# Performance work log

Measured on AMD Instinct MI355X. Metric: run time of the kernel, lower is better.

Reference implementation:

```python
import jax, jax.numpy as jnp
import numpy as np

B, S, H, D = 2, 2048, 16, 64
DM = H * D  # d_model = 1024


def setup_inputs() -> dict:
    key = jax.random.key(0)
    ks = jax.random.split(key, 12)
    scale = 1.0 / np.sqrt(DM)
    inp = {
        "queries": jax.random.normal(ks[0], (B, S, DM), jnp.float32),
        "keys": jax.random.normal(ks[1], (B, S, DM), jnp.float32),
        "values": jax.random.normal(ks[2], (B, S, DM), jnp.float32),
        # binary (0/1) causal mask, broadcast to (B, H, S, S) as the torch API expects
        "mask": jnp.broadcast_to(jnp.tril(jnp.ones((S, S), jnp.float32)), (B, H, S, S)),
        "wq": jax.random.normal(ks[3], (DM, DM), jnp.float32) * scale,
        "bq": jax.random.normal(ks[4], (DM,), jnp.float32) * scale,
        "wk": jax.random.normal(ks[5], (DM, DM), jnp.float32) * scale,
        "bk": jax.random.normal(ks[6], (DM,), jnp.float32) * scale,
        "wv": jax.random.normal(ks[7], (DM, DM), jnp.float32) * scale,
        "bv": jax.random.normal(ks[8], (DM,), jnp.float32) * scale,
        "wy": jax.random.normal(ks[9], (DM, DM), jnp.float32) * scale,
        "by": jax.random.normal(ks[10], (DM,), jnp.float32) * scale,
    }
    return inp


def _split_heads(x):
    # (B, S, H*D) -> (B, H, S, D)
    b, s, _ = x.shape
    return x.reshape(b, s, H, D).transpose(0, 2, 1, 3)


def reference(queries, keys, values, mask, wq, bq, wk, bk, wv, bv, wy, by):
    # torch nn.Linear: y = x @ W^T + b
    q = _split_heads(queries @ wq.T + bq)  # (B, H, S, D)
    k = _split_heads(keys @ wk.T + bk)
    v = _split_heads(values @ wv.T + bv)

    s = jnp.einsum("bhqd,bhkd->bhqk", q, k) / jnp.sqrt(jnp.float32(D))
    # custom additive-multiplicative mask: s*mask - 1e4*(1-mask)
    s = s * mask - 1e4 * (1.0 - mask)
    w = jax.nn.softmax(s, axis=-1)
    av = jnp.einsum("bhqk,bhkd->bhqd", w, v)  # (B, H, S, D)
    y = av.transpose(0, 2, 1, 3).reshape(queries.shape[0], queries.shape[1], DM)
    return y @ wy.T + by
```

## Files before the change

kernel.cpp:

```cpp
#include <hip/hip_runtime.h>
#include <math.h>

#define BB 2
#define SS 2048
#define HH 16
#define DD 64
#define DMODEL 1024
#define MROWS (BB * SS)

typedef __attribute__((ext_vector_type(8))) short bf16x8;
typedef __attribute__((ext_vector_type(4))) float f32x4;

__device__ __forceinline__ f32x4 mfma16(bf16x8 a, bf16x8 b, f32x4 c) {
    return __builtin_amdgcn_mfma_f32_16x16x32_bf16(a, b, c, 0, 0, 0);
}

__device__ __forceinline__ unsigned short bf16_1(float x) {
    unsigned u = __builtin_bit_cast(unsigned, x);
    u += 0x7fffu + ((u >> 16) & 1u);
    return (unsigned short)(u >> 16);
}
__device__ __forceinline__ unsigned pack_bf16(float a, float b) {
    unsigned ua = __builtin_bit_cast(unsigned, a);
    unsigned ub = __builtin_bit_cast(unsigned, b);
    ua += 0x7fffu + ((ua >> 16) & 1u);
    ub += 0x7fffu + ((ub >> 16) & 1u);
    return (ua >> 16) | (ub & 0xffff0000u);
}

__global__ __launch_bounds__(256) void cvt_bf16(const float* __restrict__ q,
                                                const float* __restrict__ k,
                                                const float* __restrict__ v,
                                                const float* __restrict__ wq,
                                                const float* __restrict__ wk,
                                                const float* __restrict__ wv,
                                                const float* __restrict__ wy,
                                                unsigned short* __restrict__ dst)
{
    const size_t idx = ((size_t)blockIdx.x * 256 + threadIdx.x) * 8;
    const int mc = (int)(idx >> 20);
    const float* src; size_t off;
    if      (mc < 4)   { src = q;  off = idx; }
    else if (mc < 8)   { src = k;  off = idx - ((size_t)4  << 20); }
    else if (mc < 12)  { src = v;  off = idx - ((size_t)8  << 20); }
    else if (mc == 12) { src = wq; off = idx - ((size_t)12 << 20); }
    else if (mc == 13) { src = wk; off = idx - ((size_t)13 << 20); }
    else if (mc == 14) { src = wv; off = idx - ((size_t)14 << 20); }
    else               { src = wy; off = idx - ((size_t)15 << 20); }
    float4 a = *(const float4*)(src + off);
    float4 b = *(const float4*)(src + off + 4);
    uint4 o;
    o.x = pack_bf16(a.x, a.y); o.y = pack_bf16(a.z, a.w);
    o.z = pack_bf16(b.x, b.y); o.w = pack_bf16(b.z, b.w);
    *(uint4*)(dst + idx) = o;
}

template<int TM>
__device__ __forceinline__ void gemm_body(const unsigned short* __restrict__ A,
                                          const unsigned short* __restrict__ W,
                                          const float* __restrict__ bias,
                                          void* __restrict__ out,
                                          int a_mode, int out_mode)
{
    constexpr int NT  = (TM == 128) ? 4 : 2;
    constexpr int ACH = TM * 8;
    __shared__ int4 lds4[ACH + 1024];
    const int tid = threadIdx.x;
    const int w = tid >> 6, lane = tid & 63;
    const int L = lane & 15, Q = lane >> 4;
    const int m0 = blockIdx.x * TM;
    const int n0 = blockIdx.y * 128;
    const int wm = (TM == 128) ? (w & 1) * 64 : 0;
    const int wn = (TM == 128) ? (w >> 1) * 64 : w * 32;

    f32x4 acc[4][NT] = {};

    for (int c = 0; c < 16; ++c) {
        __syncthreads();
        #pragma unroll
        for (int i = 0; i < TM / 32; ++i) {
            int cid = tid + 256 * i;
            int row = cid >> 3, ch = cid & 7;
            int m = m0 + row;
            size_t gaddr;
            if (a_mode == 0) gaddr = (size_t)m * DMODEL + (size_t)c * 64 + ch * 8;
            else {
                int b = m >> 11, s = m & 2047;
                gaddr = (((size_t)b * HH + c) * SS + s) * DD + ch * 8;
            }
            lds4[row * 8 + (ch ^ (row & 7))] = *(const int4*)(A + gaddr);
        }
        #pragma unroll
        for (int i = 0; i < 4; ++i) {
            int cid = tid + 256 * i;
            int row = cid >> 3, ch = cid & 7;
            lds4[ACH + row * 8 + (ch ^ (row & 7))] =
                *(const int4*)(W + (size_t)(n0 + row) * DMODEL + (size_t)c * 64 + ch * 8);
        }
        __syncthreads();
        #pragma unroll
        for (int kf = 0; kf < 2; ++kf) {
            bf16x8 af[4], bfr[NT];
            #pragma unroll
            for (int mt = 0; mt < 4; ++mt) {
                int row = wm + 16 * mt + L;
                af[mt] = __builtin_bit_cast(bf16x8, lds4[row * 8 + ((Q + 4 * kf) ^ (row & 7))]);
            }
            #pragma unroll
            for (int nt = 0; nt < NT; ++nt) {
                int row = wn + 16 * nt + L;
                bfr[nt] = __builtin_bit_cast(bf16x8, lds4[ACH + row * 8 + ((Q + 4 * kf) ^ (row & 7))]);
            }
            #pragma unroll
            for (int mt = 0; mt < 4; ++mt)
                #pragma unroll
                for (int nt = 0; nt < NT; ++nt)
                    acc[mt][nt] = mfma16(af[mt], bfr[nt], acc[mt][nt]);
        }
    }

    #pragma unroll
    for (int mt = 0; mt < 4; ++mt)
        #pragma unroll
        for (int nt = 0; nt < NT; ++nt) {
            const int mbase = m0 + wm + 16 * mt + 4 * Q;
            const int n = n0 + wn + 16 * nt + L;
            float v0 = acc[mt][nt][0] + bias[n];
            float v1 = acc[mt][nt][1] + bias[n];
            float v2 = acc[mt][nt][2] + bias[n];
            float v3 = acc[mt][nt][3] + bias[n];
            if (out_mode == 1) {
                float* o = (float*)out + (size_t)mbase * DMODEL + n;
                o[0] = v0; o[DMODEL] = v1; o[2 * DMODEL] = v2; o[3 * DMODEL] = v3;
            } else if (out_mode == 0) {
                int b = mbase >> 11, s = mbase & 2047, h = n >> 6, d = n & 63;
                unsigned short* o = (unsigned short*)out + (((size_t)b * HH + h) * SS + s) * DD + d;
                o[0] = bf16_1(v0); o[DD] = bf16_1(v1); o[2 * DD] = bf16_1(v2); o[3 * DD] = bf16_1(v3);
            } else {
                int b = mbase >> 11, s = mbase & 2047, h = n >> 6, d = n & 63;
                uint2 p; p.x = pack_bf16(v0, v1); p.y = pack_bf16(v2, v3);
                *(uint2*)((unsigned short*)out + (((size_t)b * HH + h) * DD + d) * SS + s) = p;
            }
        }
}

__global__ __launch_bounds__(256) void qkv_gemm(const unsigned short* __restrict__ qcv,
                                                const unsigned short* __restrict__ kcv,
                                                const unsigned short* __restrict__ vcv,
                                                const unsigned short* __restrict__ wqb,
                                                const unsigned short* __restrict__ wkb,
                                                const unsigned short* __restrict__ wvb,
                                                const float* __restrict__ bq,
                                                const float* __restrict__ bk,
                                                const float* __restrict__ bv,
                                                unsigned short* __restrict__ qh,
                                                unsigned short* __restrict__ kh,
                                                unsigned short* __restrict__ vtb)
{
    const int z = blockIdx.z;
    const unsigned short* A = (z == 0) ? qcv : (z == 1) ? kcv : vcv;
    const unsigned short* W = (z == 0) ? wqb : (z == 1) ? wkb : wvb;
    const float* bias       = (z == 0) ? bq  : (z == 1) ? bk  : bv;
    unsigned short* out     = (z == 0) ? qh  : (z == 1) ? kh  : vtb;
    gemm_body<128>(A, W, bias, out, 0, (z == 2) ? 2 : 0);
}

__global__ __launch_bounds__(256) void out_gemm(const unsigned short* __restrict__ avb,
                                                const unsigned short* __restrict__ wyb,
                                                const float* __restrict__ by,
                                                float* __restrict__ out)
{
    gemm_body<64>(avb, wyb, by, out, 1, 1);
}

__global__ __launch_bounds__(256) void attn_mfma(const unsigned short* __restrict__ qb,
                                                 const unsigned short* __restrict__ kb,
                                                 const unsigned short* __restrict__ vt,
                                                 unsigned short* __restrict__ av)
{
    __shared__ int4 lds4[1536];
    const int tid  = threadIdx.x;
    const int w    = tid >> 6;
    const int lane = tid & 63;
    const int L = lane & 15, Q = lane >> 4;
    const int h = blockIdx.y, b = blockIdx.z;
    const size_t base = ((size_t)b * HH + h) * SS * DD;
    const float SC = 0.125f * 1.4426950408889634f;

    const int srcA = L + 32 * (Q & 1);
    const int srcB = srcA + 16;
    const bool hisel = (Q & 2) != 0;

    for (int pass = 0; pass < 2; ++pass) {
        const int qt  = pass ? (31 - (int)blockIdx.x) : (int)blockIdx.x;
        const int q0  = qt * 64;
        const int q0w = q0 + 16 * w;

        __syncthreads();
        #pragma unroll
        for (int i = 0; i < 2; ++i) {
            int cid = tid + 256 * i;
            int row = cid >> 3, ch = cid & 7;
            lds4[row * 8 + (ch ^ (row & 7))] =
                *(const int4*)(qb + base + (size_t)(q0 + row) * DD + ch * 8);
        }
        __syncthreads();

        bf16x8 qf[2];
        #pragma unroll
        for (int kf = 0; kf < 2; ++kf) {
            int row = 16 * w + L;
            qf[kf] = __builtin_bit_cast(bf16x8, lds4[row * 8 + ((Q + 4 * kf) ^ (row & 7))]);
        }

        float m2 = -1e30f, l2 = 0.f;
        f32x4 acc[4] = {};

        const int nkt = qt + 1;
        for (int kt = 0; kt < nkt; ++kt) {
            const int k0 = kt * 64;
            __syncthreads();
            #pragma unroll
            for (int i = 0; i < 2; ++i) {
                int cid = tid + 256 * i;
                int row = cid >> 3, ch = cid & 7;
                lds4[512 + row * 8 + (ch ^ (row & 7))] =
                    *(const int4*)(kb + base + (size_t)(k0 + row) * DD + ch * 8);
            }
            #pragma unroll
            for (int i = 0; i < 2; ++i) {
                int cid = tid + 256 * i;
                int row = cid >> 3, ch = cid & 7;
                lds4[1024 + row * 8 + (ch ^ (row & 7))] =
                    *(const int4*)(vt + base + (size_t)row * SS + k0 + ch * 8);
            }
            __syncthreads();

            f32x4 st[4] = {};
            #pragma unroll
            for (int kf = 0; kf < 2; ++kf) {
                bf16x8 kfr[4];
                #pragma unroll
                for (int rt = 0; rt < 4; ++rt) {
                    int row = 16 * rt + L;
                    kfr[rt] = __builtin_bit_cast(bf16x8, lds4[512 + row * 8 + ((Q + 4 * kf) ^ (row & 7))]);
                }
                #pragma unroll
                for (int rt = 0; rt < 4; ++rt)
                    st[rt] = mfma16(kfr[rt], qf[kf], st[rt]);
            }

            const bool need_mask = (k0 + 63 > q0w);
            const int qg = q0w + L;
            float mx = -1e30f;
            #pragma unroll
            for (int rt = 0; rt < 4; ++rt)
                #pragma unroll
                for (int r = 0; r < 4; ++r) {
                    float s = st[rt][r] * SC;
                    if (need_mask) {
                        int kg = k0 + 16 * rt + 4 * Q + r;
                        s = (kg > qg) ? -2e30f : s;
                    }
                    st[rt][r] = s;
                    mx = fmaxf(mx, s);
                }
            mx = fmaxf(mx, __shfl_xor(mx, 16, 64));
            mx = fmaxf(mx, __shfl_xor(mx, 32, 64));
            const float mn = fmaxf(m2, mx);
            const float alpha = exp2f(m2 - mn);
            m2 = mn;
            float ls = 0.f;
            unsigned pd[4][2];
            #pragma unroll
            for (int rt = 0; rt < 4; ++rt) {
                float p0 = exp2f(st[rt][0] - mn), p1 = exp2f(st[rt][1] - mn);
                float p2 = exp2f(st[rt][2] - mn), p3 = exp2f(st[rt][3] - mn);
                ls += (p0 + p1) + (p2 + p3);
                pd[rt][0] = pack_bf16(p0, p1);
                pd[rt][1] = pack_bf16(p2, p3);
            }
            ls += __shfl_xor(ls, 16, 64);
            ls += __shfl_xor(ls, 32, 64);
            l2 = l2 * alpha + ls;
            #pragma unroll
            for (int rt = 0; rt < 4; ++rt) acc[rt] *= alpha;

            #pragma unroll
            for (int kf = 0; kf < 2; ++kf) {
                bf16x8 vf[4];
                #pragma unroll
                for (int rt = 0; rt < 4; ++rt) {
                    int row = 16 * rt + L;
                    vf[rt] = __builtin_bit_cast(bf16x8, lds4[1024 + row * 8 + ((Q + 4 * kf) ^ (row & 7))]);
                }
                unsigned lo0 = pd[2 * kf + 0][0], lo1 = pd[2 * kf + 0][1];
                unsigned hi0 = pd[2 * kf + 1][0], hi1 = pd[2 * kf + 1][1];
                unsigned xa_lo0 = (unsigned)__shfl((int)lo0, srcA, 64);
                unsigned xa_lo1 = (unsigned)__shfl((int)lo1, srcA, 64);
                unsigned xb_lo0 = (unsigned)__shfl((int)lo0, srcB, 64);
                unsigned xb_lo1 = (unsigned)__shfl((int)lo1, srcB, 64);
                unsigned xa_hi0 = (unsigned)__shfl((int)hi0, srcA, 64);
                unsigned xa_hi1 = (unsigned)__shfl((int)hi1, srcA, 64);
                unsigned xb_hi0 = (unsigned)__shfl((int)hi0, srcB, 64);
                unsigned xb_hi1 = (unsigned)__shfl((int)hi1, srcB, 64);
                uint4 bw;
                bw.x = hisel ? xa_hi0 : xa_lo0;
                bw.y = hisel ? xa_hi1 : xa_lo1;
                bw.z = hisel ? xb_hi0 : xb_lo0;
                bw.w = hisel ? xb_hi1 : xb_lo1;
                bf16x8 pf = __builtin_bit_cast(bf16x8, bw);
                #pragma unroll
                for (int rt = 0; rt < 4; ++rt)
                    acc[rt] = mfma16(vf[rt], pf, acc[rt]);
            }
        }

        __syncthreads();
        {
            int4* ep4 = lds4 + w * 256;
            const float inv = 1.0f / l2;
            #pragma unroll
            for (int rt = 0; rt < 4; ++rt) {
                f32x4 ov = acc[rt] * inv;
                ep4[L * 16 + ((4 * rt + Q) ^ (L & 15))] = __builtin_bit_cast(int4, ov);
            }
        }
        __syncthreads();
        {
            uint2* epu = (uint2*)(lds4 + w * 256);
            #pragma unroll
            for (int i = 0; i < 8; ++i) {
                int pid = lane + 64 * i;
                int rr  = pid >> 5;
                int c   = pid & 31;
                uint2 f2 = epu[(rr * 16 + ((c >> 1) ^ (rr & 15))) * 2 + (c & 1)];
                unsigned packed = pack_bf16(__builtin_bit_cast(float, f2.x),
                                            __builtin_bit_cast(float, f2.y));
                *(unsigned*)(av + base + (size_t)(q0 + 16 * w + rr) * DD + c * 2) = packed;
            }
        }
    }
}

extern "C" void kernel_launch(void* const* d_in, const int* in_sizes, int n_in,
                              void* d_out, int out_size, void* d_ws, size_t ws_size,
                              hipStream_t stream) {
    const float* queries = (const float*)d_in[0];
    const float* keys    = (const float*)d_in[1];
    const float* values  = (const float*)d_in[2];
    const float* wq = (const float*)d_in[4];
    const float* bq = (const float*)d_in[5];
    const float* wk = (const float*)d_in[6];
    const float* bk = (const float*)d_in[7];
    const float* wv = (const float*)d_in[8];
    const float* bv = (const float*)d_in[9];
    const float* wy = (const float*)d_in[10];
    const float* by = (const float*)d_in[11];

    unsigned short* wsb = (unsigned short*)d_ws;
    const size_t M4 = (size_t)1 << 22, M1 = (size_t)1 << 20;
    unsigned short* qcv = wsb;
    unsigned short* kcv = qcv + M4;
    unsigned short* vcv = kcv + M4;
    unsigned short* wqb = vcv + M4;
    unsigned short* wkb = wqb + M1;
    unsigned short* wvb = wkb + M1;
    unsigned short* wyb = wvb + M1;
    unsigned short* qh  = wyb + M1;
    unsigned short* kh  = qh + M4;
    unsigned short* vtb = kh + M4;
    unsigned short* avb = vtb + M4;

    cvt_bf16<<<8192, 256, 0, stream>>>(queries, keys, values, wq, wk, wv, wy, qcv);

    qkv_gemm<<<dim3(MROWS / 128, DMODEL / 128, 3), 256, 0, stream>>>(
        qcv, kcv, vcv, wqb, wkb, wvb, bq, bk, bv, qh, kh, vtb);

    attn_mfma<<<dim3(16, HH, BB), 256, 0, stream>>>(qh, kh, vtb, avb);

    out_gemm<<<dim3(MROWS / 64, DMODEL / 128), 256, 0, stream>>>(avb, wyb, by, (float*)d_out);
}
```

Measured before the change: 748.6 us.

## Use direct global-to-LDS loads, smaller GEMM N tiles, and one query tile per attention block

Replaces register-staged global loads with global_load_lds direct-to-LDS copies in the GEMMs and attention, with the swizzle applied on the global-address side. GEMM N tiles shrink from 128 to 64, doubling the grid. Attention launches 32 blocks per head, each doing one query tile, instead of 16 blocks each doing a paired light and heavy tile, and skips waves whose rows are entirely masked. This raises parallelism and cuts VGPR traffic, but the attention blocks now carry uneven causal work, and the smaller tiles reuse less data.

```diff
diff --git a/kernel.cpp b/kernel.cpp
--- a/kernel.cpp
+++ b/kernel.cpp
@@ -13,6 +13,12 @@
 
 __device__ __forceinline__ f32x4 mfma16(bf16x8 a, bf16x8 b, f32x4 c) {
     return __builtin_amdgcn_mfma_f32_16x16x32_bf16(a, b, c, 0, 0, 0);
+}
+
+__device__ __forceinline__ void gld16(const void* g, void* l) {
+    __builtin_amdgcn_global_load_lds(
+        (const __attribute__((address_space(1))) void*)g,
+        (__attribute__((address_space(3))) void*)l, 16, 0, 0);
 }
 
 __device__ __forceinline__ unsigned short bf16_1(float x) {
@@ -55,49 +61,53 @@
     *(uint4*)(dst + idx) = o;
 }
 
-template<int TM>
+template<int TM, int TN>
 __device__ __forceinline__ void gemm_body(const unsigned short* __restrict__ A,
                                           const unsigned short* __restrict__ W,
                                           const float* __restrict__ bias,
                                           void* __restrict__ out,
                                           int a_mode, int out_mode)
 {
-    constexpr int NT  = (TM == 128) ? 4 : 2;
-    constexpr int ACH = TM * 8;
-    __shared__ int4 lds4[ACH + 1024];
-    const int tid = threadIdx.x;
-    const int w = tid >> 6, lane = tid & 63;
+    constexpr int NT    = (TM == 128) ? (TN / 32) : (TN / 64);
+    constexpr int ASLOT = TM * 8;
+    __shared__ int4 lds4[ASLOT + TN * 8];
+    const int tid = threadIdx.x, w = tid >> 6, lane = tid & 63;
     const int L = lane & 15, Q = lane >> 4;
-    const int m0 = blockIdx.x * TM;
-    const int n0 = blockIdx.y * 128;
+    const int m0 = blockIdx.x * TM, n0 = blockIdx.y * TN;
     const int wm = (TM == 128) ? (w & 1) * 64 : 0;
-    const int wn = (TM == 128) ? (w >> 1) * 64 : w * 32;
+    const int wn = (TM == 128) ? (w >> 1) * (16 * NT) : w * (16 * NT);
+
+    const int lrow = lane >> 3;
+    const int lch  = (lane & 7) ^ (lrow & 7);
+    const size_t astr  = (a_mode == 0) ? 2048 : 128;
+    const size_t a_off = (size_t)lrow * astr + (size_t)lch * 16;
+    const size_t w_off = (size_t)lrow * 2048 + (size_t)lch * 16;
+    const unsigned char* Ab = (const unsigned char*)A;
+    const unsigned char* Wb = (const unsigned char*)W;
 
     f32x4 acc[4][NT] = {};
 
     for (int c = 0; c < 16; ++c) {
         __syncthreads();
+        size_t abase;
+        if (a_mode == 0) abase = (size_t)m0 * 2048 + (size_t)c * 128;
+        else {
+            int b = m0 >> 11, s = m0 & 2047;
+            abase = (((size_t)b * HH + c) * SS + s) * 128;
+        }
         #pragma unroll
         for (int i = 0; i < TM / 32; ++i) {
-            int cid = tid + 256 * i;
-            int row = cid >> 3, ch = cid & 7;
-            int m = m0 + row;
-            size_t gaddr;
-            if (a_mode == 0) gaddr = (size_t)m * DMODEL + (size_t)c * 64 + ch * 8;
-            else {
-                int b = m >> 11, s = m & 2047;
-                gaddr = (((size_t)b * HH + c) * SS + s) * DD + ch * 8;
-            }
-            lds4[row * 8 + (ch ^ (row & 7))] = *(const int4*)(A + gaddr);
-        }
-        #pragma unroll
-        for (int i = 0; i < 4; ++i) {
-            int cid = tid + 256 * i;
-            int row = cid >> 3, ch = cid & 7;
-            lds4[ACH + row * 8 + (ch ^ (row & 7))] =
-                *(const int4*)(W + (size_t)(n0 + row) * DMODEL + (size_t)c * 64 + ch * 8);
+            int win = w + 4 * i;
+            gld16(Ab + abase + (size_t)win * (8 * astr) + a_off, &lds4[win * 64]);
+        }
+        const size_t wbase = (size_t)n0 * 2048 + (size_t)c * 128;
+        #pragma unroll
+        for (int i = 0; i < TN / 32; ++i) {
+            int win = w + 4 * i;
+            gld16(Wb + wbase + (size_t)win * (8 * 2048) + w_off, &lds4[ASLOT + win * 64]);
         }
         __syncthreads();
+
         #pragma unroll
         for (int kf = 0; kf < 2; ++kf) {
             bf16x8 af[4], bfr[NT];
@@ -109,7 +119,7 @@
             #pragma unroll
             for (int nt = 0; nt < NT; ++nt) {
                 int row = wn + 16 * nt + L;
-                bfr[nt] = __builtin_bit_cast(bf16x8, lds4[ACH + row * 8 + ((Q + 4 * kf) ^ (row & 7))]);
+                bfr[nt] = __builtin_bit_cast(bf16x8, lds4[ASLOT + row * 8 + ((Q + 4 * kf) ^ (row & 7))]);
             }
             #pragma unroll
             for (int mt = 0; mt < 4; ++mt)
@@ -162,7 +172,7 @@
     const unsigned short* W = (z == 0) ? wqb : (z == 1) ? wkb : wvb;
     const float* bias       = (z == 0) ? bq  : (z == 1) ? bk  : bv;
     unsigned short* out     = (z == 0) ? qh  : (z == 1) ? kh  : vtb;
-    gemm_body<128>(A, W, bias, out, 0, (z == 2) ? 2 : 0);
+    gemm_body<128, 64>(A, W, bias, out, 0, (z == 2) ? 2 : 0);
 }
 
 __global__ __launch_bounds__(256) void out_gemm(const unsigned short* __restrict__ avb,
@@ -170,7 +180,7 @@
                                                 const float* __restrict__ by,
                                                 float* __restrict__ out)
 {
-    gemm_body<64>(avb, wyb, by, out, 1, 1);
+    gemm_body<64, 64>(avb, wyb, by, out, 1, 1);
 }
 
 __global__ __launch_bounds__(256) void attn_mfma(const unsigned short* __restrict__ qb,
@@ -187,55 +197,58 @@
     const size_t base = ((size_t)b * HH + h) * SS * DD;
     const float SC = 0.125f * 1.4426950408889634f;
 
+    const unsigned char* qB = (const unsigned char*)qb;
+    const unsigned char* kB = (const unsigned char*)kb;
+    const unsigned char* vB = (const unsigned char*)vt;
+    const size_t base2 = base * 2;
+    const int lrow = lane >> 3;
+    const int lch  = (lane & 7) ^ (lrow & 7);
+    const size_t off_rc = (size_t)lrow * 128  + (size_t)lch * 16;
+    const size_t off_vt = (size_t)lrow * 4096 + (size_t)lch * 16;
+
     const int srcA = L + 32 * (Q & 1);
     const int srcB = srcA + 16;
     const bool hisel = (Q & 2) != 0;
 
-    for (int pass = 0; pass < 2; ++pass) {
-        const int qt  = pass ? (31 - (int)blockIdx.x) : (int)blockIdx.x;
-        const int q0  = qt * 64;
-        const int q0w = q0 + 16 * w;
-
+    const int qt  = 31 - (int)blockIdx.x;
+    const int q0  = qt * 64;
+    const int q0w = q0 + 16 * w;
+
+    #pragma unroll
+    for (int i = 0; i < 2; ++i) {
+        int win = w + 4 * i;
+        gld16(qB + base2 + (size_t)(q0 + 8 * win) * 128 + off_rc, &lds4[win * 64]);
+    }
+    __syncthreads();
+
+    bf16x8 qf[2];
+    #pragma unroll
+    for (int kf = 0; kf < 2; ++kf) {
+        int row = 16 * w + L;
+        qf[kf] = __builtin_bit_cast(bf16x8, lds4[row * 8 + ((Q + 4 * kf) ^ (row & 7))]);
+    }
+
+    float m2 = -1e30f, l2 = 0.f;
+    f32x4 acc[4] = {};
+
+    const int nkt = qt + 1;
+    for (int kt = 0; kt < nkt; ++kt) {
+        const int k0 = kt * 64;
         __syncthreads();
         #pragma unroll
         for (int i = 0; i < 2; ++i) {
-            int cid = tid + 256 * i;
-            int row = cid >> 3, ch = cid & 7;
-            lds4[row * 8 + (ch ^ (row & 7))] =
-                *(const int4*)(qb + base + (size_t)(q0 + row) * DD + ch * 8);
+            int win = w + 4 * i;
+            gld16(kB + base2 + (size_t)(k0 + 8 * win) * 128 + off_rc, &lds4[512 + win * 64]);
+        }
+        #pragma unroll
+        for (int i = 0; i < 2; ++i) {
+            int win = w + 4 * i;
+            gld16(vB + base2 + (size_t)(8 * win) * 4096 + (size_t)k0 * 2 + off_vt,
+                  &lds4[1024 + win * 64]);
         }
         __syncthreads();
 
-        bf16x8 qf[2];
-        #pragma unroll
-        for (int kf = 0; kf < 2; ++kf) {
-            int row = 16 * w + L;
-            qf[kf] = __builtin_bit_cast(bf16x8, lds4[row * 8 + ((Q + 4 * kf) ^ (row & 7))]);
-        }
-
-        float m2 = -1e30f, l2 = 0.f;
-        f32x4 acc[4] = {};
-
-        const int nkt = qt + 1;
-        for (int kt = 0; kt < nkt; ++kt) {
-            const int k0 = kt * 64;
-            __syncthreads();
-            #pragma unroll
-            for (int i = 0; i < 2; ++i) {
-                int cid = tid + 256 * i;
-                int row = cid >> 3, ch = cid & 7;
-                lds4[512 + row * 8 + (ch ^ (row & 7))] =
-                    *(const int4*)(kb + base + (size_t)(k0 + row) * DD + ch * 8);
-            }
-            #pragma unroll
-            for (int i = 0; i < 2; ++i) {
-                int cid = tid + 256 * i;
-                int row = cid >> 3, ch = cid & 7;
-                lds4[1024 + row * 8 + (ch ^ (row & 7))] =
-                    *(const int4*)(vt + base + (size_t)row * SS + k0 + ch * 8);
-            }
-            __syncthreads();
-
+        if (k0 <= q0w + 15) {
             f32x4 st[4] = {};
             #pragma unroll
             for (int kf = 0; kf < 2; ++kf) {
@@ -315,30 +328,30 @@
                     acc[rt] = mfma16(vf[rt], pf, acc[rt]);
             }
         }
-
-        __syncthreads();
-        {
-            int4* ep4 = lds4 + w * 256;
-            const float inv = 1.0f / l2;
-            #pragma unroll
-            for (int rt = 0; rt < 4; ++rt) {
-                f32x4 ov = acc[rt] * inv;
-                ep4[L * 16 + ((4 * rt + Q) ^ (L & 15))] = __builtin_bit_cast(int4, ov);
-            }
-        }
-        __syncthreads();
-        {
-            uint2* epu = (uint2*)(lds4 + w * 256);
-            #pragma unroll
-            for (int i = 0; i < 8; ++i) {
-                int pid = lane + 64 * i;
-                int rr  = pid >> 5;
-                int c   = pid & 31;
-                uint2 f2 = epu[(rr * 16 + ((c >> 1) ^ (rr & 15))) * 2 + (c & 1)];
-                unsigned packed = pack_bf16(__builtin_bit_cast(float, f2.x),
-                                            __builtin_bit_cast(float, f2.y));
-                *(unsigned*)(av + base + (size_t)(q0 + 16 * w + rr) * DD + c * 2) = packed;
-            }
+    }
+
+    __syncthreads();
+    {
+        int4* ep4 = lds4 + w * 256;
+        const float inv = 1.0f / l2;
+        #pragma unroll
+        for (int rt = 0; rt < 4; ++rt) {
+            f32x4 ov = acc[rt] * inv;
+            ep4[L * 16 + ((4 * rt + Q) ^ (L & 15))] = __builtin_bit_cast(int4, ov);
+        }
+    }
+    __syncthreads();
+    {
+        uint2* epu = (uint2*)(lds4 + w * 256);
+        #pragma unroll
+        for (int i = 0; i < 8; ++i) {
+            int pid = lane + 64 * i;
+            int rr  = pid >> 5;
+            int c   = pid & 31;
+            uint2 f2 = epu[(rr * 16 + ((c >> 1) ^ (rr & 15))) * 2 + (c & 1)];
+            unsigned packed = pack_bf16(__builtin_bit_cast(float, f2.x),
+                                        __builtin_bit_cast(float, f2.y));
+            *(unsigned*)(av + base + (size_t)(q0 + 16 * w + rr) * DD + c * 2) = packed;
         }
     }
 }
@@ -374,10 +387,10 @@
 
     cvt_bf16<<<8192, 256, 0, stream>>>(queries, keys, values, wq, wk, wv, wy, qcv);
 
-    qkv_gemm<<<dim3(MROWS / 128, DMODEL / 128, 3), 256, 0, stream>>>(
+    qkv_gemm<<<dim3(MROWS / 128, DMODEL / 64, 3), 256, 0, stream>>>(
         qcv, kcv, vcv, wqb, wkb, wvb, bq, bk, bv, qh, kh, vtb);
 
-    attn_mfma<<<dim3(16, HH, BB), 256, 0, stream>>>(qh, kh, vtb, avb);
-
-    out_gemm<<<dim3(MROWS / 64, DMODEL / 128), 256, 0, stream>>>(avb, wyb, by, (float*)d_out);
-}
+    attn_mfma<<<dim3(32, HH, BB), 256, 0, stream>>>(qh, kh, vtb, avb);
+
+    out_gemm<<<dim3(MROWS / 64, DMODEL / 64), 256, 0, stream>>>(avb, wyb, by, (float*)d_out);
+}
```

New measurement: 768.7 us. 1.03x slower.
